# Kernel optimization log

Hardware: AMD Instinct MI355X
Metric: run time of the kernel (lower is better)

Reference implementation:

```python
import jax, jax.numpy as jnp
import numpy as np

N, CIO, L = 16, 512, 384
DIMHEAD, NUMHEAD, MAXEMBED, DIMGROUP = 64, 8, 384, 8
CHID = DIMHEAD * NUMHEAD


def setup_inputs() -> dict:
    key = jax.random.key(0)
    ks = jax.random.split(key, 12)
    s = 0.05
    return {
        "x": jax.random.normal(ks[0], (N, CIO, L), jnp.float32),
        "xorg": jax.random.normal(ks[1], (N, CIO, L), jnp.float32),
        "abspos": jax.random.normal(ks[2], (N, CIO, L), jnp.float32),
        "mask": jnp.zeros((N, L), jnp.float32),
        "norm": jnp.full((N,), 8.0, jnp.float32),
        "qkpos_res": s * jax.random.normal(ks[3], (CIO // DIMGROUP, 1), jnp.float32),
        "qkorg_res": s * jax.random.normal(ks[4], (CIO // DIMGROUP, 1), jnp.float32),
        "vorg_res": s * jax.random.normal(ks[5], (CIO // DIMGROUP, 1), jnp.float32),
        "relpos": s * jax.random.normal(ks[6], (2 * MAXEMBED - 1,), jnp.float32),
        "gate_w": s * jax.random.normal(ks[7], (NUMHEAD, CIO), jnp.float32),
        "gate_b": jnp.zeros((NUMHEAD,), jnp.float32),
        "q_w": s * jax.random.normal(ks[8], (CHID, CIO), jnp.float32),
        "k_w": s * jax.random.normal(ks[9], (CHID, CIO), jnp.float32),
        "v_w": s * jax.random.normal(ks[10], (CHID, CIO), jnp.float32),
        "dense_w": s * jax.random.normal(ks[11], (CIO, CHID), jnp.float32),
        "dense_b": jnp.zeros((CIO,), jnp.float32),
    }


def _rezero(t, res):
    # (N,C,L) -> reshape to (N, C//DIMGROUP, DIMGROUP*L), scale per group, reshape back
    n, c, l = t.shape
    return (t.reshape(n, c // DIMGROUP, -1) * res).reshape(n, c, l)


def _relpos_idx():
    # idx[i, j] = clip(MAXEMBED - i + j, 0, 2*MAXEMBED - 2)
    idx = np.arange(MAXEMBED, MAXEMBED - L, -1)[:, None] + np.arange(L)[None, :]
    return jnp.asarray(np.clip(idx, 0, 2 * MAXEMBED - 2))


def reference(x, xorg, abspos, mask, norm, qkpos_res, qkorg_res, vorg_res,
              relpos, gate_w, gate_b, q_w, k_w, v_w, dense_w, dense_b):
    n = x.shape[0]
    x0 = x + _rezero(xorg, vorg_res)                     # value path
    x1 = x + _rezero(xorg, qkorg_res) + _rezero(abspos, qkpos_res)  # qk path

    q = jnp.einsum('oc,ncl->nol', q_w, x1).reshape(n, NUMHEAD, DIMHEAD, L)
    k = jnp.einsum('oc,ncl->nol', k_w, x1).reshape(n, NUMHEAD, DIMHEAD, L)
    v = jnp.einsum('oc,ncl->nol', v_w, x0).reshape(n, NUMHEAD, DIMHEAD, L)

    scores = jnp.einsum('nhdi,nhdj->nhij', q, k)         # (N, H, L, L)
    gate = jnp.einsum('oc,ncl->nol', gate_w, x) + gate_b[None, :, None]  # (N, H, L)
    scores = (scores + relpos[_relpos_idx()]
              + gate[:, :, None, :]
              + mask[:, None, None, :]) / norm[:, None, None, None]

    attn = jax.nn.softmax(scores, axis=-1)
    out = jnp.einsum('nhij,nhdj->nhdi', attn, v).reshape(n, CHID, L)
    out = jnp.einsum('oc,ncl->nol', dense_w, out) + dense_b[None, :, None]
    return out
```

## Files before the change

kernel.cpp:

```cpp
#include <hip/hip_runtime.h>
#include <hip/hip_bf16.h>

#define N_B   16
#define CIO   512
#define LSEQ  384
#define DH    64
#define NH    8
#define CHID  512
#define ME    384

typedef __hip_bfloat16 bf16;
typedef __attribute__((ext_vector_type(8))) short bf16x8;
typedef __attribute__((ext_vector_type(4))) float f32x4;

#define AS1 __attribute__((address_space(1)))
#define AS3 __attribute__((address_space(3)))

__device__ __forceinline__ unsigned short f2bs(float f) {
    union { bf16 b; unsigned short u; } cv; cv.b = __float2bfloat16(f); return cv.u;
}

__device__ __forceinline__ void gload_lds16(const bf16* g, bf16* l) {
    __builtin_amdgcn_global_load_lds((const AS1 unsigned int*)g,
                                     (AS3 unsigned int*)l, 16, 0, 0);
}

__launch_bounds__(256)
__global__ void prep_kernel(const float* __restrict__ x, const float* __restrict__ xorg,
                            const float* __restrict__ abspos,
                            const float* __restrict__ qkorg, const float* __restrict__ qkpos,
                            const float* __restrict__ vorg,
                            const float* __restrict__ gw,
                            const float* __restrict__ q_w, const float* __restrict__ k_w,
                            const float* __restrict__ v_w, const float* __restrict__ dense_w,
                            bf16* __restrict__ wqb, bf16* __restrict__ wkb,
                            bf16* __restrict__ wvb, bf16* __restrict__ wdb,
                            bf16* __restrict__ x1t, bf16* __restrict__ x0t,
                            float* __restrict__ gpart)
{
    __shared__ bf16 T1[64 * 72], T0[64 * 72];
    __shared__ float Traw[64 * 65];
    __shared__ float gws[NH * 64];
    __shared__ float r0[64], r1[64], r2[64];
    const int tid = threadIdx.x;
    const int cb = blockIdx.x;
    const int c0 = cb * 64;
    const int l0 = blockIdx.y * 64;
    const int n  = blockIdx.z;

    {
        int f = blockIdx.x + 8 * (blockIdx.y + 6 * blockIdx.z);
        if (f < 512) {
            int e = (f * 256 + tid) * 8;
            int which = e >> 18;
            int off = e & ((1 << 18) - 1);
            const float* s = which == 0 ? q_w : which == 1 ? k_w : which == 2 ? v_w : dense_w;
            bf16* d       = which == 0 ? wqb : which == 1 ? wkb : which == 2 ? wvb : wdb;
            float4 f0 = *(const float4*)&s[off];
            float4 f1 = *(const float4*)&s[off + 4];
            unsigned short u[8] = {f2bs(f0.x), f2bs(f0.y), f2bs(f0.z), f2bs(f0.w),
                                   f2bs(f1.x), f2bs(f1.y), f2bs(f1.z), f2bs(f1.w)};
            *(uint4*)&d[off] = *(uint4*)u;
        }
    }

    if (tid < 64) {
        int gidx = (c0 + tid) >> 3;
        r0[tid] = vorg[gidx];
        r1[tid] = qkorg[gidx];
        r2[tid] = qkpos[gidx];
    }
    for (int t = tid; t < NH * 64; t += 256) {
        int h = t >> 6, c = t & 63;
        gws[t] = gw[h * CIO + c0 + c];
    }
    __syncthreads();
    const int l = tid & 63, cs = tid >> 6;
    #pragma unroll
    for (int r = 0; r < 16; r++) {
        int cl = r * 4 + cs;
        size_t gi = ((size_t)n * CIO + c0 + cl) * LSEQ + l0 + l;
        float xv = x[gi], xo = xorg[gi];
        Traw[cl * 65 + l] = xv;
        T0[l * 72 + cl] = __float2bfloat16(xv + r0[cl] * xo);
        T1[l * 72 + cl] = __float2bfloat16(xv + r1[cl] * xo + r2[cl] * abspos[gi]);
    }
    __syncthreads();
    for (int t = tid; t < NH * 64; t += 256) {
        int h = t >> 6, ll = t & 63;
        float s = 0.f;
        #pragma unroll
        for (int c = 0; c < 64; c++) s += gws[h * 64 + c] * Traw[c * 65 + ll];
        gpart[(((size_t)cb * N_B + n) * NH + h) * LSEQ + l0 + ll] = s;
    }
    #pragma unroll
    for (int t = 0; t < 2; t++) {
        int idx = t * 256 + tid;
        int lr = idx >> 3, u = idx & 7;
        size_t go = ((size_t)n * LSEQ + l0 + lr) * CIO + c0 + u * 8;
        *(uint4*)&x1t[go] = *(const uint4*)&T1[lr * 72 + u * 8];
        *(uint4*)&x0t[go] = *(const uint4*)&T0[lr * 72 + u * 8];
    }
}

__launch_bounds__(256)
__global__ void qkv_kernel(const bf16* __restrict__ wall,
                           const bf16* __restrict__ x1t, const bf16* __restrict__ x0t,
                           bf16* __restrict__ qb, bf16* __restrict__ kb,
                           bf16* __restrict__ vb)
{
    __shared__ __align__(16) char smem[17408];
    bf16* As = (bf16*)smem;
    bf16* Bs = (bf16*)(smem + 8192);
    bf16* S  = (bf16*)smem;

    const int tid = threadIdx.x;
    const int lane = tid & 63, w = tid >> 6;
    const int l15 = lane & 15, g = lane >> 4;
    const int Bid = blockIdx.x;
    const int rres = Bid & 7, qq = Bid >> 3;
    const int n = rres + 8 * (qq / 36);
    const int t = qq % 36;
    const int ot = t / 3;
    const int lt = t % 3;
    const int osub = (w & 1) * 64, lsub = (w >> 1) * 64;

    const bf16* Wt = wall + (size_t)(ot * 128) * CIO;
    const bf16* Bt = (ot < 8 ? x1t : x0t) + ((size_t)n * LSEQ + lt * 128) * CIO;

    const int segA = 2 * w, segB = 2 * w + 1;
    const int eA = segA * 512 + lane * 8;
    const int eB = segB * 512 + lane * 8;
    const int rA = eA >> 5, cA = eA & 31;
    const int rB = eB >> 5, cB = eB & 31;

    f32x4 acc[4][4];
    #pragma unroll
    for (int mt = 0; mt < 4; mt++)
        #pragma unroll
        for (int jt = 0; jt < 4; jt++) acc[mt][jt] = f32x4{0.f, 0.f, 0.f, 0.f};

    for (int it = 0; it < 16; ++it) {
        const int k0 = it * 32;
        gload_lds16(Wt + (size_t)rA * CIO + k0 + cA, As + segA * 512);
        gload_lds16(Wt + (size_t)rB * CIO + k0 + cB, As + segB * 512);
        gload_lds16(Bt + (size_t)rA * CIO + k0 + cA, Bs + segA * 512);
        gload_lds16(Bt + (size_t)rB * CIO + k0 + cB, Bs + segB * 512);
        __syncthreads();
        bf16x8 af[4], bfv[4];
        #pragma unroll
        for (int mt = 0; mt < 4; mt++)
            af[mt] = *(const bf16x8*)&As[(osub + mt * 16 + l15) * 32 + 8 * g];
        #pragma unroll
        for (int jt = 0; jt < 4; jt++)
            bfv[jt] = *(const bf16x8*)&Bs[(lsub + jt * 16 + l15) * 32 + 8 * g];
        #pragma unroll
        for (int mt = 0; mt < 4; mt++)
            #pragma unroll
            for (int jt = 0; jt < 4; jt++)
                acc[mt][jt] = __builtin_amdgcn_mfma_f32_16x16x32_bf16(af[mt], bfv[jt], acc[mt][jt], 0, 0, 0);
        __syncthreads();
    }

    if (ot < 8) {
        bf16* dstb = (ot < 4) ? qb : kb;
        const int hbase = 2 * (ot & 3);
        #pragma unroll
        for (int lh = 0; lh < 2; ++lh) {
            if ((w >> 1) == lh) {
                #pragma unroll
                for (int mt = 0; mt < 4; mt++)
                    #pragma unroll
                    for (int jt = 0; jt < 4; jt++)
                        #pragma unroll
                        for (int r = 0; r < 4; r++)
                            S[(jt * 16 + l15) * 136 + osub + mt * 16 + 4 * g + r] =
                                __float2bfloat16(acc[mt][jt][r]);
            }
            __syncthreads();
            #pragma unroll
            for (int t2 = 0; t2 < 4; ++t2) {
                int idx = t2 * 256 + tid;
                int lr = idx >> 4, u = idx & 15;
                int ho = u >> 3, dc = u & 7;
                bf16* dst = dstb + (((size_t)n * NH + hbase + ho) * LSEQ
                                    + lt * 128 + lh * 64 + lr) * DH + dc * 8;
                *(uint4*)dst = *(const uint4*)&S[lr * 136 + u * 8];
            }
            __syncthreads();
        }
    } else {
        const int ob = (ot - 8) * 128;
        #pragma unroll
        for (int oh = 0; oh < 2; ++oh) {
            if ((w & 1) == oh) {
                #pragma unroll
                for (int mt = 0; mt < 4; mt++)
                    #pragma unroll
                    for (int jt = 0; jt < 4; jt++)
                        #pragma unroll
                        for (int r = 0; r < 4; r++)
                            S[(mt * 16 + 4 * g + r) * 136 + lsub + jt * 16 + l15] =
                                __float2bfloat16(acc[mt][jt][r]);
            }
            __syncthreads();
            #pragma unroll
            for (int t2 = 0; t2 < 4; ++t2) {
                int idx = t2 * 256 + tid;
                int orr = idx >> 4, u = idx & 15;
                bf16* dst = vb + ((size_t)(n * CHID + ob + oh * 64 + orr)) * LSEQ
                               + lt * 128 + u * 8;
                *(uint4*)dst = *(const uint4*)&S[orr * 136 + u * 8];
            }
            __syncthreads();
        }
    }
}

#define KVT 64
#define NT  (LSEQ / KVT)

__launch_bounds__(256, 3)
__global__ void attn_kernel(const bf16* __restrict__ qt,
                            const bf16* __restrict__ kt,
                            const bf16* __restrict__ v,
                            const float* __restrict__ gpart,
                            const float* __restrict__ gb,
                            const float* __restrict__ mask,
                            const float* __restrict__ norm,
                            const float* __restrict__ relpos,
                            bf16* __restrict__ ctxt)
{
    __shared__ __align__(16) bf16 Kb[2][KVT * DH];
    __shared__ __align__(16) bf16 Vb[2][KVT * DH];
    __shared__ __align__(16) bf16 P[4 * 16 * 64];
    __shared__ float relp_s[2 * ME - 1];
    __shared__ float radd_s[LSEQ];

    const int tid = threadIdx.x;
    const int Bid = blockIdx.x;
    const int rres = Bid & 7, qq = Bid >> 3;
    const int n = rres + 8 * (qq / 48);
    const int rem = qq % 48;
    const int h = rem / 6;
    const int i0 = (rem % 6) * 64;
    const int lane = tid & 63;
    const int w = tid >> 6;
    const int l15 = lane & 15, g = lane >> 4;
    const int m0 = w * 16;

    const size_t nh = (size_t)n * NH + h;
    const bf16* kt_g = kt + nh * LSEQ * DH;
    const bf16* vg   = v + ((size_t)n * CHID + h * DH) * LSEQ;

    {
        const float gbh = gb[h];
        for (int i = tid; i < LSEQ; i += 256) {
            float s = gbh + mask[(size_t)n * LSEQ + i];
            #pragma unroll
            for (int cb = 0; cb < 8; cb++)
                s += gpart[(((size_t)cb * N_B + n) * NH + h) * LSEQ + i];
            radd_s[i] = s;
        }
    }
    for (int i = tid; i < 2 * ME - 1; i += 256) relp_s[i] = relpos[i];

    const bf16* qrow = qt + (nh * LSEQ + i0 + m0 + l15) * DH;
    bf16x8 a0 = *(const bf16x8*)&qrow[8 * g];
    bf16x8 a1 = *(const bf16x8*)&qrow[8 * g + 32];
    const float inv_norm = 1.0f / norm[n];

    const int c0_ = (2 * w) * 64 + lane;
    const int c1_ = (2 * w + 1) * 64 + lane;
    const int kr0 = c0_ >> 3, kc0 = ((c0_ & 7) ^ (kr0 & 7)) * 8;
    const int kr1 = c1_ >> 3, kc1 = ((c1_ & 7) ^ (kr1 & 7)) * 8;
    const int koff0 = kr0 * DH + kc0, koff1 = kr1 * DH + kc1;
    const int voff0 = kr0 * LSEQ + kc0, voff1 = kr1 * LSEQ + kc1;

    gload_lds16(kt_g + koff0, &Kb[0][(2 * w) * 512]);
    gload_lds16(kt_g + koff1, &Kb[0][(2 * w + 1) * 512]);
    gload_lds16(vg + voff0, &Vb[0][(2 * w) * 512]);
    gload_lds16(vg + voff1, &Vb[0][(2 * w + 1) * 512]);
    __syncthreads();

    const int ib = i0 + m0 + 4 * g;
    bf16* Pw = P + w * 1024;

    f32x4 oacc[4];
    #pragma unroll
    for (int dn = 0; dn < 4; dn++) oacc[dn] = f32x4{0.f, 0.f, 0.f, 0.f};
    float m_r[4]  = {-1e30f, -1e30f, -1e30f, -1e30f};
    float lsum[4] = {0.f, 0.f, 0.f, 0.f};

    #pragma unroll 2
    for (int t = 0; t < NT; ++t) {
        const int cur = t & 1;
        if (t + 1 < NT) {
            const bf16* kn = kt_g + (t + 1) * (KVT * DH);
            const bf16* vn = vg + (t + 1) * KVT;
            gload_lds16(kn + koff0, &Kb[cur ^ 1][(2 * w) * 512]);
            gload_lds16(kn + koff1, &Kb[cur ^ 1][(2 * w + 1) * 512]);
            gload_lds16(vn + voff0, &Vb[cur ^ 1][(2 * w) * 512]);
            gload_lds16(vn + voff1, &Vb[cur ^ 1][(2 * w + 1) * 512]);
        }

        f32x4 acc[4];
        #pragma unroll
        for (int jt = 0; jt < 4; jt++) acc[jt] = f32x4{0.f, 0.f, 0.f, 0.f};
        #pragma unroll
        for (int jt = 0; jt < 4; jt++) {
            const int row = jt * 16 + l15;
            bf16x8 b0 = *(const bf16x8*)&Kb[cur][row * 64 + ((g ^ (row & 7)) * 8)];
            bf16x8 b1 = *(const bf16x8*)&Kb[cur][row * 64 + (((4 + g) ^ (row & 7)) * 8)];
            acc[jt] = __builtin_amdgcn_mfma_f32_16x16x32_bf16(a0, b0, acc[jt], 0, 0, 0);
            acc[jt] = __builtin_amdgcn_mfma_f32_16x16x32_bf16(a1, b1, acc[jt], 0, 0, 0);
        }

        float mx[4] = {-1e30f, -1e30f, -1e30f, -1e30f};
        #pragma unroll
        for (int jt = 0; jt < 4; jt++) {
            const int j = t * KVT + jt * 16 + l15;
            const float ra = radd_s[j];
            const int idxb = ME - ib + j;
            #pragma unroll
            for (int r = 0; r < 4; r++) {
                int idx = idxb - r;
                idx = (idx > 2 * ME - 2) ? (2 * ME - 2) : idx;
                float s = (acc[jt][r] + relp_s[idx] + ra) * inv_norm;
                acc[jt][r] = s;
                mx[r] = fmaxf(mx[r], s);
            }
        }
        #pragma unroll
        for (int r = 0; r < 4; r++) {
            #pragma unroll
            for (int off = 1; off <= 8; off <<= 1)
                mx[r] = fmaxf(mx[r], __shfl_xor(mx[r], off));
            float mnew = fmaxf(m_r[r], mx[r]);
            float sc = __expf(m_r[r] - mnew);
            m_r[r] = mnew;
            lsum[r] *= sc;
            #pragma unroll
            for (int dn = 0; dn < 4; dn++) oacc[dn][r] *= sc;
        }
        #pragma unroll
        for (int jt = 0; jt < 4; jt++) {
            const int col = jt * 16 + l15;
            #pragma unroll
            for (int r = 0; r < 4; r++) {
                const int lr = 4 * g + r;
                float e = __expf(acc[jt][r] - m_r[r]);
                lsum[r] += e;
                Pw[lr * 64 + (col ^ ((lr & 7) << 3))] = __float2bfloat16(e);
            }
        }

        #pragma unroll
        for (int kh = 0; kh < 2; kh++) {
            bf16x8 a = *(const bf16x8*)&Pw[l15 * 64 + (((kh * 4 + g) ^ (l15 & 7)) * 8)];
            #pragma unroll
            for (int dn = 0; dn < 4; dn++) {
                const int vr = dn * 16 + l15;
                bf16x8 bv = *(const bf16x8*)&Vb[cur][vr * 64 + (((kh * 4 + g) ^ (vr & 7)) * 8)];
                oacc[dn] = __builtin_amdgcn_mfma_f32_16x16x32_bf16(a, bv, oacc[dn], 0, 0, 0);
            }
        }
        __syncthreads();
    }

    float rs[4];
    #pragma unroll
    for (int r = 0; r < 4; r++) {
        float tm = lsum[r];
        #pragma unroll
        for (int off = 1; off <= 8; off <<= 1) tm += __shfl_xor(tm, off);
        rs[r] = 1.0f / tm;
    }

    bf16* O = &Kb[0][0];
    #pragma unroll
    for (int dn = 0; dn < 4; dn++)
        #pragma unroll
        for (int r = 0; r < 4; r++)
            O[(m0 + 4 * g + r) * 72 + dn * 16 + l15] = __float2bfloat16(oacc[dn][r] * rs[r]);
    __syncthreads();

    bf16* cg_ = ctxt + ((size_t)n * LSEQ + i0) * CHID + h * DH;
    #pragma unroll
    for (int t = 0; t < 2; t++) {
        int idx = t * 256 + tid;
        int ir = idx >> 3, u = idx & 7;
        *(uint4*)&cg_[(size_t)ir * CHID + u * 8] = *(const uint4*)&O[ir * 72 + u * 8];
    }
}

__launch_bounds__(256, 6)
__global__ void dense_kernel(const bf16* __restrict__ Wb,
                             const bf16* __restrict__ Bt,
                             const float* __restrict__ bias,
                             float* __restrict__ outf)
{
    __shared__ __align__(16) float S[64 * 68];
    const int tid = threadIdx.x;
    const int lane = tid & 63, w = tid >> 6;
    const int l15 = lane & 15, g = lane >> 4;
    const int Bid = blockIdx.x;
    const int rres = Bid & 7, qq = Bid >> 3;
    const int n = rres + 8 * (qq / 48);
    const int tt = qq % 48;
    const int o0 = (tt / 6) * 64;
    const int l0 = (tt % 6) * 64;

    const bf16* arow = Wb + (size_t)(o0 + l15) * CIO + 8 * g;
    const bf16* brow = Bt + ((size_t)n * LSEQ + l0 + w * 16 + l15) * CIO + 8 * g;

    f32x4 acc[4];
    #pragma unroll
    for (int mt = 0; mt < 4; mt++) acc[mt] = f32x4{0.f, 0.f, 0.f, 0.f};
    #pragma unroll 4
    for (int it = 0; it < 16; it++) {
        const int k0 = it * 32;
        bf16x8 b = *(const bf16x8*)&brow[k0];
        bf16x8 a[4];
        #pragma unroll
        for (int mt = 0; mt < 4; mt++)
            a[mt] = *(const bf16x8*)&arow[(size_t)mt * 16 * CIO + k0];
        #pragma unroll
        for (int mt = 0; mt < 4; mt++)
            acc[mt] = __builtin_amdgcn_mfma_f32_16x16x32_bf16(a[mt], b, acc[mt], 0, 0, 0);
    }

    #pragma unroll
    for (int mt = 0; mt < 4; mt++)
        #pragma unroll
        for (int r = 0; r < 4; r++)
            S[(mt * 16 + 4 * g + r) * 68 + w * 16 + l15] =
                acc[mt][r] + bias[o0 + mt * 16 + 4 * g + r];
    __syncthreads();
    float* og = outf + ((size_t)n * CHID + o0) * LSEQ + l0;
    #pragma unroll
    for (int t = 0; t < 4; t++) {
        int idx = t * 256 + tid;
        int orow = idx >> 4, u = idx & 15;
        *(float4*)&og[(size_t)orow * LSEQ + u * 4] = *(const float4*)&S[orow * 68 + u * 4];
    }
}

extern "C" void kernel_launch(void* const* d_in, const int* in_sizes, int n_in,
                              void* d_out, int out_size, void* d_ws, size_t ws_size,
                              hipStream_t stream)
{
    const float* x       = (const float*)d_in[0];
    const float* xorg    = (const float*)d_in[1];
    const float* abspos  = (const float*)d_in[2];
    const float* mask    = (const float*)d_in[3];
    const float* norm    = (const float*)d_in[4];
    const float* qkpos   = (const float*)d_in[5];
    const float* qkorg   = (const float*)d_in[6];
    const float* vorg    = (const float*)d_in[7];
    const float* relpos  = (const float*)d_in[8];
    const float* gate_w  = (const float*)d_in[9];
    const float* gate_b  = (const float*)d_in[10];
    const float* q_w     = (const float*)d_in[11];
    const float* k_w     = (const float*)d_in[12];
    const float* v_w     = (const float*)d_in[13];
    const float* dense_w = (const float*)d_in[14];
    const float* dense_b = (const float*)d_in[15];
    float* out = (float*)d_out;

    const size_t TEN = (size_t)N_B * CHID * LSEQ * sizeof(bf16);
    const size_t WB  = (size_t)CHID * CIO * sizeof(bf16);
    char* ws = (char*)d_ws;
    bf16*  x1t  = (bf16*)(ws);
    bf16*  x0t  = (bf16*)(ws + TEN);
    bf16*  qb   = (bf16*)(ws + 2 * TEN);
    bf16*  kb   = (bf16*)(ws + 3 * TEN);
    bf16*  vb   = (bf16*)(ws + 4 * TEN);
    bf16*  wqb  = (bf16*)(ws + 5 * TEN);
    bf16*  wkb  = (bf16*)(ws + 5 * TEN + WB);
    bf16*  wvb  = (bf16*)(ws + 5 * TEN + 2 * WB);
    bf16*  wdb  = (bf16*)(ws + 5 * TEN + 3 * WB);
    float* gpart = (float*)(ws + 5 * TEN + 4 * WB);
    bf16*  ctxt = x1t;

    prep_kernel<<<dim3(CIO / 64, LSEQ / 64, N_B), 256, 0, stream>>>(
        x, xorg, abspos, qkorg, qkpos, vorg, gate_w,
        q_w, k_w, v_w, dense_w, wqb, wkb, wvb, wdb, x1t, x0t, gpart);
    qkv_kernel<<<576, 256, 0, stream>>>(wqb, x1t, x0t, qb, kb, vb);
    attn_kernel<<<768, 256, 0, stream>>>(qb, kb, vb, gpart, gate_b,
                                         mask, norm, relpos, ctxt);
    dense_kernel<<<768, 256, 0, stream>>>(wdb, ctxt, dense_b, out);
}
```

Before: 178.7 us.

## Move gate projection to MFMA blocks in QKV kernel and double-buffer QKV loads

The scalar fp32 gate projection in the prep kernel and its 8-way partial sum in attention are removed. Instead, prep writes a bf16 transposed copy of x, and 16 extra QKV blocks compute the gate through MFMA using a zero-padded bf16 gate weight. The QKV GEMM main loop is also double-buffered in LDS, so the next k-tile loads while the current one is computed. In exchange, prep writes one more bf16 tensor, LDS use grows to 32KB per block, and the gate is now computed at bf16 precision.

```diff
diff --git a/kernel.cpp b/kernel.cpp
--- a/kernel.cpp
+++ b/kernel.cpp
@@ -30,17 +30,16 @@
                             const float* __restrict__ abspos,
                             const float* __restrict__ qkorg, const float* __restrict__ qkpos,
                             const float* __restrict__ vorg,
-                            const float* __restrict__ gw,
+                            const float* __restrict__ gate_w,
                             const float* __restrict__ q_w, const float* __restrict__ k_w,
                             const float* __restrict__ v_w, const float* __restrict__ dense_w,
                             bf16* __restrict__ wqb, bf16* __restrict__ wkb,
                             bf16* __restrict__ wvb, bf16* __restrict__ wdb,
+                            bf16* __restrict__ wgb,
                             bf16* __restrict__ x1t, bf16* __restrict__ x0t,
-                            float* __restrict__ gpart)
+                            bf16* __restrict__ xrt)
 {
-    __shared__ bf16 T1[64 * 72], T0[64 * 72];
-    __shared__ float Traw[64 * 65];
-    __shared__ float gws[NH * 64];
+    __shared__ bf16 T1[64 * 72], T0[64 * 72], TR[64 * 72];
     __shared__ float r0[64], r1[64], r2[64];
     const int tid = threadIdx.x;
     const int cb = blockIdx.x;
@@ -61,6 +60,21 @@
             unsigned short u[8] = {f2bs(f0.x), f2bs(f0.y), f2bs(f0.z), f2bs(f0.w),
                                    f2bs(f1.x), f2bs(f1.y), f2bs(f1.z), f2bs(f1.w)};
             *(uint4*)&d[off] = *(uint4*)u;
+        } else if (f == 512) {
+            int e = tid * 16;
+            float4 f0 = *(const float4*)&gate_w[e];
+            float4 f1 = *(const float4*)&gate_w[e + 4];
+            float4 f2 = *(const float4*)&gate_w[e + 8];
+            float4 f3 = *(const float4*)&gate_w[e + 12];
+            unsigned short u[16] = {f2bs(f0.x), f2bs(f0.y), f2bs(f0.z), f2bs(f0.w),
+                                    f2bs(f1.x), f2bs(f1.y), f2bs(f1.z), f2bs(f1.w),
+                                    f2bs(f2.x), f2bs(f2.y), f2bs(f2.z), f2bs(f2.w),
+                                    f2bs(f3.x), f2bs(f3.y), f2bs(f3.z), f2bs(f3.w)};
+            *(uint4*)&wgb[e]     = *(uint4*)&u[0];
+            *(uint4*)&wgb[e + 8] = *(uint4*)&u[8];
+            uint4 z = {0u, 0u, 0u, 0u};
+            *(uint4*)&wgb[4096 + e]     = z;
+            *(uint4*)&wgb[4096 + e + 8] = z;
         }
     }
 
@@ -70,10 +84,6 @@
         r1[tid] = qkorg[gidx];
         r2[tid] = qkpos[gidx];
     }
-    for (int t = tid; t < NH * 64; t += 256) {
-        int h = t >> 6, c = t & 63;
-        gws[t] = gw[h * CIO + c0 + c];
-    }
     __syncthreads();
     const int l = tid & 63, cs = tid >> 6;
     #pragma unroll
@@ -81,18 +91,11 @@
         int cl = r * 4 + cs;
         size_t gi = ((size_t)n * CIO + c0 + cl) * LSEQ + l0 + l;
         float xv = x[gi], xo = xorg[gi];
-        Traw[cl * 65 + l] = xv;
+        TR[l * 72 + cl] = __float2bfloat16(xv);
         T0[l * 72 + cl] = __float2bfloat16(xv + r0[cl] * xo);
         T1[l * 72 + cl] = __float2bfloat16(xv + r1[cl] * xo + r2[cl] * abspos[gi]);
     }
     __syncthreads();
-    for (int t = tid; t < NH * 64; t += 256) {
-        int h = t >> 6, ll = t & 63;
-        float s = 0.f;
-        #pragma unroll
-        for (int c = 0; c < 64; c++) s += gws[h * 64 + c] * Traw[c * 65 + ll];
-        gpart[(((size_t)cb * N_B + n) * NH + h) * LSEQ + l0 + ll] = s;
-    }
     #pragma unroll
     for (int t = 0; t < 2; t++) {
         int idx = t * 256 + tid;
@@ -100,18 +103,21 @@
         size_t go = ((size_t)n * LSEQ + l0 + lr) * CIO + c0 + u * 8;
         *(uint4*)&x1t[go] = *(const uint4*)&T1[lr * 72 + u * 8];
         *(uint4*)&x0t[go] = *(const uint4*)&T0[lr * 72 + u * 8];
+        *(uint4*)&xrt[go] = *(const uint4*)&TR[lr * 72 + u * 8];
     }
 }
 
 __launch_bounds__(256)
 __global__ void qkv_kernel(const bf16* __restrict__ wall,
+                           const bf16* __restrict__ wgb,
                            const bf16* __restrict__ x1t, const bf16* __restrict__ x0t,
+                           const bf16* __restrict__ xrt,
                            bf16* __restrict__ qb, bf16* __restrict__ kb,
-                           bf16* __restrict__ vb)
+                           bf16* __restrict__ vb, float* __restrict__ gateb)
 {
-    __shared__ __align__(16) char smem[17408];
+    __shared__ __align__(16) char smem[32768];
     bf16* As = (bf16*)smem;
-    bf16* Bs = (bf16*)(smem + 8192);
+    bf16* Bs = (bf16*)(smem + 16384);
     bf16* S  = (bf16*)smem;
 
     const int tid = threadIdx.x;
@@ -119,8 +125,34 @@
     const int l15 = lane & 15, g = lane >> 4;
     const int Bid = blockIdx.x;
     const int rres = Bid & 7, qq = Bid >> 3;
-    const int n = rres + 8 * (qq / 36);
-    const int t = qq % 36;
+    const int n = rres + 8 * (qq / 37);
+    const int t = qq % 37;
+
+    if (t == 36) {
+        const bf16* xr = xrt + (size_t)n * LSEQ * CIO;
+        const int colbase = w * 96;
+        f32x4 ac[6];
+        #pragma unroll
+        for (int jt = 0; jt < 6; jt++) ac[jt] = f32x4{0.f, 0.f, 0.f, 0.f};
+        for (int it = 0; it < 16; ++it) {
+            const int k0 = it * 32;
+            bf16x8 a = *(const bf16x8*)&wgb[(size_t)l15 * CIO + k0 + 8 * g];
+            #pragma unroll
+            for (int jt = 0; jt < 6; jt++) {
+                bf16x8 b = *(const bf16x8*)&xr[(size_t)(colbase + jt * 16 + l15) * CIO + k0 + 8 * g];
+                ac[jt] = __builtin_amdgcn_mfma_f32_16x16x32_bf16(a, b, ac[jt], 0, 0, 0);
+            }
+        }
+        if (g < 2) {
+            #pragma unroll
+            for (int jt = 0; jt < 6; jt++)
+                #pragma unroll
+                for (int r = 0; r < 4; r++)
+                    gateb[((size_t)n * NH + 4 * g + r) * LSEQ + colbase + jt * 16 + l15] = ac[jt][r];
+        }
+        return;
+    }
+
     const int ot = t / 3;
     const int lt = t % 3;
     const int osub = (w & 1) * 64, lsub = (w >> 1) * 64;
@@ -140,20 +172,32 @@
         #pragma unroll
         for (int jt = 0; jt < 4; jt++) acc[mt][jt] = f32x4{0.f, 0.f, 0.f, 0.f};
 
+    gload_lds16(Wt + (size_t)rA * CIO + cA, As + segA * 512);
+    gload_lds16(Wt + (size_t)rB * CIO + cB, As + segB * 512);
+    gload_lds16(Bt + (size_t)rA * CIO + cA, Bs + segA * 512);
+    gload_lds16(Bt + (size_t)rB * CIO + cB, Bs + segB * 512);
+    __syncthreads();
+
     for (int it = 0; it < 16; ++it) {
-        const int k0 = it * 32;
-        gload_lds16(Wt + (size_t)rA * CIO + k0 + cA, As + segA * 512);
-        gload_lds16(Wt + (size_t)rB * CIO + k0 + cB, As + segB * 512);
-        gload_lds16(Bt + (size_t)rA * CIO + k0 + cA, Bs + segA * 512);
-        gload_lds16(Bt + (size_t)rB * CIO + k0 + cB, Bs + segB * 512);
-        __syncthreads();
+        const int cur = it & 1;
+        if (it < 15) {
+            const int k1 = (it + 1) * 32;
+            bf16* Ad = As + (cur ^ 1) * 4096;
+            bf16* Bd = Bs + (cur ^ 1) * 4096;
+            gload_lds16(Wt + (size_t)rA * CIO + k1 + cA, Ad + segA * 512);
+            gload_lds16(Wt + (size_t)rB * CIO + k1 + cB, Ad + segB * 512);
+            gload_lds16(Bt + (size_t)rA * CIO + k1 + cA, Bd + segA * 512);
+            gload_lds16(Bt + (size_t)rB * CIO + k1 + cB, Bd + segB * 512);
+        }
+        const bf16* Ac = As + cur * 4096;
+        const bf16* Bc = Bs + cur * 4096;
         bf16x8 af[4], bfv[4];
         #pragma unroll
         for (int mt = 0; mt < 4; mt++)
-            af[mt] = *(const bf16x8*)&As[(osub + mt * 16 + l15) * 32 + 8 * g];
+            af[mt] = *(const bf16x8*)&Ac[(osub + mt * 16 + l15) * 32 + 8 * g];
         #pragma unroll
         for (int jt = 0; jt < 4; jt++)
-            bfv[jt] = *(const bf16x8*)&Bs[(lsub + jt * 16 + l15) * 32 + 8 * g];
+            bfv[jt] = *(const bf16x8*)&Bc[(lsub + jt * 16 + l15) * 32 + 8 * g];
         #pragma unroll
         for (int mt = 0; mt < 4; mt++)
             #pragma unroll
@@ -224,7 +268,7 @@
 __global__ void attn_kernel(const bf16* __restrict__ qt,
                             const bf16* __restrict__ kt,
                             const bf16* __restrict__ v,
-                            const float* __restrict__ gpart,
+                            const float* __restrict__ gateb,
                             const float* __restrict__ gb,
                             const float* __restrict__ mask,
                             const float* __restrict__ norm,
@@ -255,13 +299,9 @@
 
     {
         const float gbh = gb[h];
-        for (int i = tid; i < LSEQ; i += 256) {
-            float s = gbh + mask[(size_t)n * LSEQ + i];
-            #pragma unroll
-            for (int cb = 0; cb < 8; cb++)
-                s += gpart[(((size_t)cb * N_B + n) * NH + h) * LSEQ + i];
-            radd_s[i] = s;
-        }
+        const float* gr = gateb + nh * LSEQ;
+        for (int i = tid; i < LSEQ; i += 256)
+            radd_s[i] = gbh + mask[(size_t)n * LSEQ + i] + gr[i];
     }
     for (int i = tid; i < 2 * ME - 1; i += 256) relp_s[i] = relpos[i];
 
@@ -480,14 +520,16 @@
     bf16*  wkb  = (bf16*)(ws + 5 * TEN + WB);
     bf16*  wvb  = (bf16*)(ws + 5 * TEN + 2 * WB);
     bf16*  wdb  = (bf16*)(ws + 5 * TEN + 3 * WB);
-    float* gpart = (float*)(ws + 5 * TEN + 4 * WB);
+    bf16*  wgb  = (bf16*)(ws + 5 * TEN + 4 * WB);
+    float* gateb = (float*)(ws + 5 * TEN + 4 * WB + 16384);
+    bf16*  xrt  = (bf16*)(ws + 5 * TEN + 4 * WB + 16384 + 196608);
     bf16*  ctxt = x1t;
 
     prep_kernel<<<dim3(CIO / 64, LSEQ / 64, N_B), 256, 0, stream>>>(
         x, xorg, abspos, qkorg, qkpos, vorg, gate_w,
-        q_w, k_w, v_w, dense_w, wqb, wkb, wvb, wdb, x1t, x0t, gpart);
-    qkv_kernel<<<576, 256, 0, stream>>>(wqb, x1t, x0t, qb, kb, vb);
-    attn_kernel<<<768, 256, 0, stream>>>(qb, kb, vb, gpart, gate_b,
+        q_w, k_w, v_w, dense_w, wqb, wkb, wvb, wdb, wgb, x1t, x0t, xrt);
+    qkv_kernel<<<592, 256, 0, stream>>>(wqb, wgb, x1t, x0t, xrt, qb, kb, vb, gateb);
+    attn_kernel<<<768, 256, 0, stream>>>(qb, kb, vb, gateb, gate_b,
                                          mask, norm, relpos, ctxt);
     dense_kernel<<<768, 256, 0, stream>>>(wdb, ctxt, dense_b, out);
 }
```

New measurement: 192.3 us. 7.6% more time.
